# Performance work log

Hardware: AMD Instinct MI355X
Metric: run time of the kernel (lower is better)

Reference implementation:

```python
import jax, jax.numpy as jnp
import numpy as np

BATCH = 8192
IN_F = 1024
OUT_F = 1024
GRID_SIZE = 5
SPLINE_ORDER = 3
GRID_LO, GRID_HI = -1.0, 1.0


def setup_inputs() -> dict:
    key = jax.random.key(0)
    k1, k2, k3, k4 = jax.random.split(key, 4)
    x = jax.random.normal(k1, (BATCH, IN_F), dtype=jnp.float32)
    # grid buffer: extended knot vector, same for every input feature
    h = (GRID_HI - GRID_LO) / GRID_SIZE
    knots = jnp.linspace(GRID_LO - SPLINE_ORDER * h, GRID_HI + SPLINE_ORDER * h,
                         GRID_SIZE + 2 * SPLINE_ORDER + 1, dtype=jnp.float32)
    grid = jnp.tile(knots[None, :], (IN_F, 1))  # [in, 12]
    fan_in_scale = 1.0 / np.sqrt(IN_F)
    base_weight = jax.random.normal(k2, (OUT_F, IN_F), dtype=jnp.float32) * fan_in_scale
    spline_weight = jax.random.normal(k3, (IN_F, GRID_SIZE + SPLINE_ORDER, OUT_F), dtype=jnp.float32) * 0.1
    spline_scaler = jax.random.normal(k4, (IN_F, OUT_F), dtype=jnp.float32) * fan_in_scale
    return {"x": x, "grid": grid, "base_weight": base_weight,
            "spline_weight": spline_weight, "spline_scaler": spline_scaler}


def b_splines(x, grid):
    """Cox-de Boor recursion. x: [B, in], grid: [in, G+2k+1] -> [B, in, G+k]."""
    xe = x[:, :, None]  # [B, in, 1]
    bases = ((xe >= grid[:, :-1]) & (xe < grid[:, 1:])).astype(x.dtype)  # [B, in, G+2k]
    for k in range(1, SPLINE_ORDER + 1):
        left = (xe - grid[:, :-(k + 1)]) / (grid[:, k:-1] - grid[:, :-(k + 1)])
        right = (grid[:, k + 1:] - xe) / (grid[:, k + 1:] - grid[:, 1:-k])
        bases = left * bases[:, :, :-1] + right * bases[:, :, 1:]
    return bases  # [B, in, G+k]


def reference(x, grid, base_weight, spline_weight, spline_scaler):
    # base branch: SiLU(x) @ W_base^T
    base_out = jax.nn.silu(x) @ base_weight.T  # [B, out]
    # spline branch
    basis = b_splines(x, grid)  # [B, in, G+k]
    scaled_w = spline_weight * spline_scaler[:, None, :]  # [in, G+k, out]
    spline_out = jnp.einsum('bik,iko->bo', basis, scaled_w)  # [B, out]
    return base_out + spline_out
```

## Files before the change

### kernel.cpp

```cpp
#include <hip/hip_runtime.h>
#include <cstdint>
#include <cstddef>

#define BATCH 8192
#define IN_F 1024
#define OUT_F 1024
#define NSPL 9
#define KDIM (IN_F * NSPL)

#define BM 256
#define BN 256
#define KS (KDIM / 2)
#define NH (KS / 32)

typedef __bf16 bf16x8 __attribute__((ext_vector_type(8)));
typedef float f32x4 __attribute__((ext_vector_type(4)));

__device__ __forceinline__ void g2l16(const void* g, void* l) {
  __builtin_amdgcn_global_load_lds(
      (__attribute__((address_space(1))) void*)(g),
      (__attribute__((address_space(3))) void*)(l),
      16, 0, 0);
}

__device__ __forceinline__ void barrier_raw() {
  asm volatile("" ::: "memory");
  __builtin_amdgcn_s_barrier();
  asm volatile("" ::: "memory");
}

__global__ __launch_bounds__(256) void build_w(const float* __restrict__ bw,
                                               const float* __restrict__ sw,
                                               const float* __restrict__ sc,
                                               __bf16* __restrict__ Wt) {
  __shared__ float s_sw[16 * 8 * 64];
  __shared__ float s_sc[16 * 64];
  __shared__ float s_bw[64 * 16];
  __shared__ __align__(16) __bf16 s_out[64 * 144];
  const int tid = threadIdx.x;
  const int o0 = (blockIdx.x & 15) * 64;
  const int i0 = (blockIdx.x >> 4) * 16;

#pragma unroll
  for (int it = 0; it < 32; ++it) {
    const int t = it * 256 + tid;
    const int i = t >> 9, r = (t >> 6) & 7, oo = t & 63;
    s_sw[t] = sw[((size_t)(i0 + i) * 8 + r) * OUT_F + o0 + oo];
  }
#pragma unroll
  for (int it = 0; it < 4; ++it) {
    const int t = it * 256 + tid;
    const int i = t >> 6, oo = t & 63;
    s_sc[t] = sc[(size_t)(i0 + i) * OUT_F + o0 + oo];
  }
#pragma unroll
  for (int it = 0; it < 4; ++it) {
    const int t = it * 256 + tid;
    const int oo = t >> 4, ii = t & 15;
    s_bw[t] = bw[(size_t)(o0 + oo) * IN_F + i0 + ii];
  }
  __syncthreads();

  const int oo = tid >> 2;
  const int isub = (tid & 3) * 4;
#pragma unroll
  for (int is = 0; is < 4; ++is) {
    const int i = isub + is;
    __bf16* dst = s_out + oo * 144 + i * 9;
    dst[0] = (__bf16)s_bw[oo * 16 + i];
    const float scal = s_sc[i * 64 + oo];
#pragma unroll
    for (int r = 0; r < 8; ++r)
      dst[1 + r] = (__bf16)(s_sw[i * 512 + r * 64 + oo] * scal);
  }
  __syncthreads();

  const uint2* s2 = (const uint2*)s_out;
#pragma unroll
  for (int k = 0; k < 9; ++k) {
    const int idx = k * 256 + tid;
    const int row = idx / 36;
    const int col = idx - row * 36;
    *(uint2*)(Wt + (size_t)(o0 + row) * KDIM + (size_t)i0 * 9 + col * 4) = s2[idx];
  }
}

__global__ __launch_bounds__(256) void build_a(const float* __restrict__ x,
                                               __bf16* __restrict__ A) {
  __shared__ __align__(16) __bf16 rowbuf[2 * KDIM];
  const int tid = threadIdx.x;
  const int r2 = tid >> 7;
  const int tr = tid & 127;
  const size_t b = (size_t)blockIdx.x * 2 + r2;

  const float4* xp = (const float4*)(x + b * IN_F + (size_t)tr * 8);
  const float4 v0 = xp[0], v1 = xp[1];
  const float vv[8] = {v0.x, v0.y, v0.z, v0.w, v1.x, v1.y, v1.z, v1.w};

  union HB { __bf16 h[72]; uint4 q[9]; } hb;

#pragma unroll
  for (int f = 0; f < 8; ++f) {
    const float v = vv[f];
    const float s0 = v / (1.f + __expf(-v));
    const float p = (v + 2.2f) * 2.5f;
    const int cell = (int)floorf(p);
    const bool ok = (cell >= 0) && (cell <= 10) && (v < 2.2f);
    const float gate = ok ? (1.f / 6.f) : 0.f;
    const float t = p - (float)cell;
    const float t2 = t * t, t3 = t2 * t;
    const float omt = 1.f - t;
    const float c0 = gate * omt * omt * omt;
    const float c1 = gate * (3.f * t3 - 6.f * t2 + 4.f);
    const float c2 = gate * (-3.f * t3 + 3.f * t2 + 3.f * t + 1.f);
    const float c3 = gate * t3;
    const int j0 = cell - 3;
    hb.h[f * 9 + 0] = (__bf16)s0;
#pragma unroll
    for (int r = 0; r < 8; ++r) {
      const int d = r - j0;
      float val = (d == 0) ? c0 : 0.f;
      val = (d == 1) ? c1 : val;
      val = (d == 2) ? c2 : val;
      val = (d == 3) ? c3 : val;
      hb.h[f * 9 + 1 + r] = (__bf16)val;
    }
  }

  uint4* ldst = (uint4*)(rowbuf + (size_t)r2 * KDIM) + (size_t)tr * 9;
#pragma unroll
  for (int k = 0; k < 9; ++k) ldst[k] = hb.q[k];
  __syncthreads();

  const uint4* src = (const uint4*)rowbuf;
  uint4* dst = (uint4*)(A + (size_t)blockIdx.x * 2 * KDIM);
#pragma unroll
  for (int it = 0; it < 9; ++it)
    dst[it * 256 + tid] = src[it * 256 + tid];
}

__global__ __launch_bounds__(512, 2) void gemm_bt(const __bf16* __restrict__ A,
                                                  const __bf16* __restrict__ W,
                                                  float* __restrict__ out,
                                                  float* __restrict__ part) {
  __shared__ __align__(16) __bf16 As[4][BM * 32];
  __shared__ __align__(16) __bf16 Bs[4][BN * 32];

  const int tid = threadIdx.x;
  const int wv = tid >> 6;
  const int lane = tid & 63;

  const int bid = blockIdx.x;
  const int xcd = bid & 7;
  const int j = bid >> 3;
  const int m0 = (xcd * 4 + (j & 3)) * BM;
  const int n0 = ((j >> 2) & 3) * BN;
  const int ks = j >> 4;
  const size_t kbase = (size_t)ks * KS;

  const int wr = wv >> 2;
  const int wc = wv & 3;

  const int srow = lane >> 2;
  const int usrc = (lane & 3) ^ ((lane >> 3) & 3);
  const __bf16* gA = A + (size_t)(m0 + wv * 32 + srow) * KDIM + kbase + usrc * 8;
  const __bf16* gB = W + (size_t)(n0 + wv * 32 + srow) * KDIM + kbase + usrc * 8;

#define STAGE_HALF(s, hh)                                             \
  do {                                                                \
    const size_t ko = (size_t)(hh) * 32;                              \
    g2l16(gA + ko,                     &As[s][wv * 1024]);            \
    g2l16(gA + ko + 16 * (size_t)KDIM, &As[s][wv * 1024 + 512]);      \
    g2l16(gB + ko,                     &Bs[s][wv * 1024]);            \
    g2l16(gB + ko + 16 * (size_t)KDIM, &Bs[s][wv * 1024 + 512]);      \
  } while (0)

  const int mrow = lane & 15;
  const int quad = lane >> 4;
  const int xu = (quad ^ ((mrow >> 1) & 3)) * 8;
  int aoff[8], boff[4];
#pragma unroll
  for (int mt = 0; mt < 8; ++mt) aoff[mt] = (wr * 128 + mt * 16 + mrow) * 32 + xu;
#pragma unroll
  for (int nt = 0; nt < 4; ++nt) boff[nt] = (wc * 64 + nt * 16 + mrow) * 32 + xu;

  f32x4 acc[8][4];
  const f32x4 zero = {0.f, 0.f, 0.f, 0.f};
#pragma unroll
  for (int mt = 0; mt < 8; ++mt)
#pragma unroll
    for (int nt = 0; nt < 4; ++nt) acc[mt][nt] = zero;

  STAGE_HALF(0, 0);
  STAGE_HALF(1, 1);
  STAGE_HALF(2, 2);
  asm volatile("s_waitcnt vmcnt(8)" ::: "memory");
  barrier_raw();

  for (int h = 0; h < NH; ++h) {
    const int s = h & 3;

    bf16x8 af[4], bf[4];
#pragma unroll
    for (int mt = 0; mt < 4; ++mt) af[mt] = *(const bf16x8*)(&As[s][aoff[mt]]);
#pragma unroll
    for (int nt = 0; nt < 4; ++nt) bf[nt] = *(const bf16x8*)(&Bs[s][boff[nt]]);

    if (h + 3 < NH) {
      STAGE_HALF((h + 3) & 3, h + 3);
      asm volatile("s_waitcnt vmcnt(8)" ::: "memory");
    } else if (h + 2 < NH) {
      asm volatile("s_waitcnt vmcnt(4)" ::: "memory");
    } else {
      asm volatile("s_waitcnt vmcnt(0)" ::: "memory");
    }
    barrier_raw();

    __builtin_amdgcn_s_setprio(1);
#pragma unroll
    for (int mt = 0; mt < 4; ++mt)
#pragma unroll
      for (int nt = 0; nt < 4; ++nt)
        acc[mt][nt] = __builtin_amdgcn_mfma_f32_16x16x32_bf16(af[mt], bf[nt],
                                                              acc[mt][nt], 0, 0, 0);
    __builtin_amdgcn_s_setprio(0);
    barrier_raw();

    bf16x8 af2[4];
#pragma unroll
    for (int mt = 0; mt < 4; ++mt) af2[mt] = *(const bf16x8*)(&As[s][aoff[4 + mt]]);
    barrier_raw();

    __builtin_amdgcn_s_setprio(1);
#pragma unroll
    for (int mt = 0; mt < 4; ++mt)
#pragma unroll
      for (int nt = 0; nt < 4; ++nt)
        acc[4 + mt][nt] = __builtin_amdgcn_mfma_f32_16x16x32_bf16(af2[mt], bf[nt],
                                                                  acc[4 + mt][nt],
                                                                  0, 0, 0);
    __builtin_amdgcn_s_setprio(0);
    barrier_raw();
  }

  float* __restrict__ dst = ks ? part : out;
#pragma unroll
  for (int mt = 0; mt < 8; ++mt) {
#pragma unroll
    for (int nt = 0; nt < 4; ++nt) {
      const int col = n0 + wc * 64 + nt * 16 + mrow;
      const int rbase = m0 + wr * 128 + mt * 16 + quad * 4;
#pragma unroll
      for (int r = 0; r < 4; ++r)
        dst[(size_t)(rbase + r) * OUT_F + col] = acc[mt][nt][r];
    }
  }
#undef STAGE_HALF
}

__global__ __launch_bounds__(256) void reduce_add(float* __restrict__ out,
                                                  const float* __restrict__ part) {
  const size_t base = (size_t)blockIdx.x * 256 + threadIdx.x;
  f32x4* o = (f32x4*)out;
  const f32x4* p = (const f32x4*)part;
#pragma unroll
  for (int it = 0; it < 4; ++it) {
    const size_t i = base + (size_t)it * 2048 * 256;
    f32x4 a = o[i], b = p[i];
    a.x += b.x; a.y += b.y; a.z += b.z; a.w += b.w;
    o[i] = a;
  }
}

extern "C" void kernel_launch(void* const* d_in, const int* in_sizes, int n_in,
                              void* d_out, int out_size, void* d_ws, size_t ws_size,
                              hipStream_t stream) {
  const float* x  = (const float*)d_in[0];
  const float* bw = (const float*)d_in[2];
  const float* sw = (const float*)d_in[3];
  const float* sc = (const float*)d_in[4];
  float* out = (float*)d_out;

  __bf16* Wt = (__bf16*)d_ws;
  __bf16* Ab = (__bf16*)((char*)d_ws +
                         (size_t)OUT_F * KDIM * sizeof(__bf16));
  float* part = (float*)((char*)d_ws +
                         (size_t)OUT_F * KDIM * sizeof(__bf16) +
                         (size_t)BATCH * KDIM * sizeof(__bf16));

  build_w<<<1024, 256, 0, stream>>>(bw, sw, sc, Wt);
  build_a<<<BATCH / 2, 256, 0, stream>>>(x, Ab);
  gemm_bt<<<(BATCH / BM) * (OUT_F / BN) * 2, 512, 0, stream>>>(Ab, Wt, out, part);
  reduce_add<<<2048, 256, 0, stream>>>(out, part);
}
```

Baseline: 307.4 us.

## Restructure GEMM main loop to process two K-slices per barrier with paired staging

Replaces the per-slice loop, which had four barriers and a 3-deep prefetch, with a loop that handles two K-slices per iteration. Each iteration loads all A/B fragments for a slice, issues loads for the next two slices into the free buffers, runs all 32 MFMAs, repeats for the second slice, then waits for vmcnt(0) once and hits a single barrier. The goal is to cut barrier and wait overhead and to give the scheduler larger MFMA blocks. The cost is shallower prefetch, since each wait now drains all outstanding loads, and higher register pressure from holding 8 A fragments at once.

```diff
diff --git a/kernel.cpp b/kernel.cpp
--- a/kernel.cpp
+++ b/kernel.cpp
@@ -12,6 +12,7 @@
 #define BN 256
 #define KS (KDIM / 2)
 #define NH (KS / 32)
+#define NSP (NH / 2)
 
 typedef __bf16 bf16x8 __attribute__((ext_vector_type(8)));
 typedef float f32x4 __attribute__((ext_vector_type(4)));
@@ -193,53 +194,50 @@
 
   STAGE_HALF(0, 0);
   STAGE_HALF(1, 1);
-  STAGE_HALF(2, 2);
-  asm volatile("s_waitcnt vmcnt(8)" ::: "memory");
+  asm volatile("s_waitcnt vmcnt(0)" ::: "memory");
   barrier_raw();
 
-  for (int h = 0; h < NH; ++h) {
-    const int s = h & 3;
-
-    bf16x8 af[4], bf[4];
-#pragma unroll
-    for (int mt = 0; mt < 4; ++mt) af[mt] = *(const bf16x8*)(&As[s][aoff[mt]]);
-#pragma unroll
-    for (int nt = 0; nt < 4; ++nt) bf[nt] = *(const bf16x8*)(&Bs[s][boff[nt]]);
-
-    if (h + 3 < NH) {
-      STAGE_HALF((h + 3) & 3, h + 3);
-      asm volatile("s_waitcnt vmcnt(8)" ::: "memory");
-    } else if (h + 2 < NH) {
-      asm volatile("s_waitcnt vmcnt(4)" ::: "memory");
-    } else {
-      asm volatile("s_waitcnt vmcnt(0)" ::: "memory");
-    }
-    barrier_raw();
+  for (int p = 0; p < NSP; ++p) {
+    const int w0 = 2 * p;
+    const int s0 = w0 & 3;
+    const int s1 = (w0 + 1) & 3;
+    const int d0 = (w0 + 2) & 3;
+    const int d1 = (w0 + 3) & 3;
+
+    bf16x8 af[8], bf[4];
+#pragma unroll
+    for (int mt = 0; mt < 8; ++mt) af[mt] = *(const bf16x8*)(&As[s0][aoff[mt]]);
+#pragma unroll
+    for (int nt = 0; nt < 4; ++nt) bf[nt] = *(const bf16x8*)(&Bs[s0][boff[nt]]);
+
+    if (w0 + 2 < NH) STAGE_HALF(d0, w0 + 2);
+    if (w0 + 3 < NH) STAGE_HALF(d1, w0 + 3);
 
     __builtin_amdgcn_s_setprio(1);
 #pragma unroll
-    for (int mt = 0; mt < 4; ++mt)
+    for (int mt = 0; mt < 8; ++mt)
 #pragma unroll
       for (int nt = 0; nt < 4; ++nt)
         acc[mt][nt] = __builtin_amdgcn_mfma_f32_16x16x32_bf16(af[mt], bf[nt],
                                                               acc[mt][nt], 0, 0, 0);
     __builtin_amdgcn_s_setprio(0);
-    barrier_raw();
-
-    bf16x8 af2[4];
-#pragma unroll
-    for (int mt = 0; mt < 4; ++mt) af2[mt] = *(const bf16x8*)(&As[s][aoff[4 + mt]]);
-    barrier_raw();
+
+    bf16x8 af2[8], bf2[4];
+#pragma unroll
+    for (int mt = 0; mt < 8; ++mt) af2[mt] = *(const bf16x8*)(&As[s1][aoff[mt]]);
+#pragma unroll
+    for (int nt = 0; nt < 4; ++nt) bf2[nt] = *(const bf16x8*)(&Bs[s1][boff[nt]]);
 
     __builtin_amdgcn_s_setprio(1);
 #pragma unroll
-    for (int mt = 0; mt < 4; ++mt)
+    for (int mt = 0; mt < 8; ++mt)
 #pragma unroll
       for (int nt = 0; nt < 4; ++nt)
-        acc[4 + mt][nt] = __builtin_amdgcn_mfma_f32_16x16x32_bf16(af2[mt], bf[nt],
-                                                                  acc[4 + mt][nt],
-                                                                  0, 0, 0);
+        acc[mt][nt] = __builtin_amdgcn_mfma_f32_16x16x32_bf16(af2[mt], bf2[nt],
+                                                              acc[mt][nt], 0, 0, 0);
     __builtin_amdgcn_s_setprio(0);
+
+    asm volatile("s_waitcnt vmcnt(0)" ::: "memory");
     barrier_raw();
   }
 
```

New measurement: 290.6 us. -5.5%, faster.
